# Kernel tuning notes

Measured on AMD Instinct MI355X. Metric: run time of the kernel, lower is better.

## Reference

```python
import jax, jax.numpy as jnp
import numpy as np

THRESHOLD = 0.5
NEGPOS_RATIO = 3
VARIANCES = (0.1, 0.2)

B, P, C, T = 64, 24564, 81, 50


def point_form(boxes):
    # center form (cx,cy,w,h) -> corner form (x1,y1,x2,y2)
    return jnp.concatenate([boxes[:, :2] - boxes[:, 2:] / 2,
                            boxes[:, :2] + boxes[:, 2:] / 2], axis=-1)


def jaccard(box_a, box_b):
    # box_a [T,4], box_b [P,4], corner form -> IoU [T,P]
    max_xy = jnp.minimum(box_a[:, None, 2:], box_b[None, :, 2:])
    min_xy = jnp.maximum(box_a[:, None, :2], box_b[None, :, :2])
    inter = jnp.prod(jnp.clip(max_xy - min_xy, 0.0), axis=-1)
    area_a = jnp.prod(box_a[:, 2:] - box_a[:, :2], axis=-1)[:, None]
    area_b = jnp.prod(box_b[:, 2:] - box_b[:, :2], axis=-1)[None, :]
    return inter / (area_a + area_b - inter)


def encode(matched, priors, variances):
    # matched [P,4] corner form, priors [P,4] center form
    g_cxcy = (matched[:, :2] + matched[:, 2:]) / 2 - priors[:, :2]
    g_cxcy = g_cxcy / (variances[0] * priors[:, 2:])
    g_wh = (matched[:, 2:] - matched[:, :2]) / priors[:, 2:]
    g_wh = jnp.log(g_wh) / variances[1]
    return jnp.concatenate([g_cxcy, g_wh], axis=-1)


def match_one(truths, labels, priors):
    # truths [T,4] corner, labels [T] int, priors [P,4] center form
    overlaps = jaccard(truths, point_form(priors))          # [T,P]
    best_prior_idx = jnp.argmax(overlaps, axis=1)           # [T] best prior per gt
    best_truth_overlap = jnp.max(overlaps, axis=0)          # [P]
    best_truth_idx = jnp.argmax(overlaps, axis=0)           # [P]
    # ensure every gt keeps its best prior
    best_truth_overlap = best_truth_overlap.at[best_prior_idx].set(2.0)
    best_truth_idx = best_truth_idx.at[best_prior_idx].set(jnp.arange(truths.shape[0]))
    matched = truths[best_truth_idx]                        # [P,4]
    conf = labels[best_truth_idx] + 1                       # background = 0
    conf = jnp.where(best_truth_overlap < THRESHOLD, 0, conf)
    loc = encode(matched, priors, VARIANCES)                # [P,4]
    return loc, conf


def setup_inputs() -> dict:
    key = jax.random.key(0)
    k1, k2, k3, k4, k5, k6, k7 = jax.random.split(key, 7)
    loc_data = jax.random.normal(k1, (B, P, 4), jnp.float32)
    conf_data = jax.random.normal(k2, (B, P, C), jnp.float32)
    # priors: center form, in-bounds
    ctr = 0.05 + 0.9 * jax.random.uniform(k3, (P, 2))
    wh = 0.05 + 0.25 * jax.random.uniform(k4, (P, 2))
    priors = jnp.concatenate([ctr, wh], axis=-1).astype(jnp.float32)
    # gt boxes: corner form with x2>x1, y2>y1
    xy1 = 0.7 * jax.random.uniform(k5, (B, T, 2))
    gwh = 0.05 + 0.25 * jax.random.uniform(k6, (B, T, 2))
    targets_boxes = jnp.concatenate([xy1, jnp.minimum(xy1 + gwh, 1.0)], axis=-1).astype(jnp.float32)
    targets_labels = jax.random.randint(k7, (B, T), 0, C - 1, jnp.int32)
    return {"loc_data": loc_data, "conf_data": conf_data, "priors": priors,
            "targets_boxes": targets_boxes, "targets_labels": targets_labels}


def reference(loc_data, conf_data, priors, targets_boxes, targets_labels):
    num, num_priors, _ = loc_data.shape
    # per-image matching, batched with vmap
    loc_t, conf_t = jax.vmap(lambda t, l: match_one(t, l, priors))(targets_boxes, targets_labels)
    pos = conf_t > 0                                         # [B,P]
    # localization: smooth-L1 over positives, sum
    diff = loc_data - loc_t
    ad = jnp.abs(diff)
    sl1 = jnp.where(ad < 1.0, 0.5 * diff * diff, ad - 0.5)
    loss_l = jnp.sum(sl1 * pos[..., None])
    # confidence: cross entropy = logsumexp - gathered logit
    logsm = jax.nn.log_softmax(conf_data, axis=-1)
    ce = -jnp.take_along_axis(logsm, conf_t[..., None], axis=-1)[..., 0]  # [B,P]
    # hard negative mining: rank losses among negatives
    loss_mine = jnp.where(pos, 0.0, ce)
    num_pos = jnp.sum(pos, axis=1)                           # [B]
    num_neg = jnp.minimum(NEGPOS_RATIO * num_pos, num_priors - 1)
    idx_rank = jnp.argsort(jnp.argsort(-loss_mine, axis=1), axis=1)
    neg = idx_rank < num_neg[:, None]
    loss_c = jnp.sum(jnp.where(pos | neg, ce, 0.0))
    n = jnp.maximum(jnp.sum(num_pos), 1).astype(loc_data.dtype)
    return jnp.stack([loss_l / n, loss_c / n])
```

## Files before the change

kernel.cpp:

```cpp
#include <hip/hip_runtime.h>
#include <cstdint>
#include <cstddef>

#define NB 64
#define NP 24564
#define NC 81
#define NROWS (NB*NP)
#define NT 50
#define TCH 10
#define NSEG 16
#define SEGLEN 1536

__device__ __forceinline__ unsigned long long umax64(unsigned long long a, unsigned long long b){
  return a > b ? a : b;
}

__global__ __launch_bounds__(256) void k_bestprior(
    const float* __restrict__ priors, const float* __restrict__ tboxes,
    unsigned long long* __restrict__ bpk)
{
  __shared__ float tb[TCH*4];
  __shared__ float ta[TCH];
  __shared__ unsigned long long part[4][TCH];
  const int tid = threadIdx.x;
  const int b  = blockIdx.x;
  const int t0 = blockIdx.y * TCH;
  const int i0 = blockIdx.z * SEGLEN;
  const int iend = min(i0 + SEGLEN, NP);
  if (tid < TCH*4) tb[tid] = tboxes[(b*NT + t0)*4 + tid];
  __syncthreads();
  if (tid < TCH) ta[tid] = (tb[tid*4+2]-tb[tid*4+0]) * (tb[tid*4+3]-tb[tid*4+1]);
  __syncthreads();

  unsigned long long best[TCH];
  #pragma unroll
  for (int j = 0; j < TCH; ++j) best[j] = 0ULL;

  for (int i = i0 + tid; i < iend; i += 256){
    const float4 pr = ((const float4* __restrict__)priors)[i];
    const float px1 = pr.x - 0.5f*pr.z, py1 = pr.y - 0.5f*pr.w;
    const float px2 = pr.x + 0.5f*pr.z, py2 = pr.y + 0.5f*pr.w;
    const float pa  = pr.z * pr.w;
    const unsigned long long low = (unsigned long long)(~(unsigned)i);
    #pragma unroll
    for (int j = 0; j < TCH; ++j){
      float ix = fminf(tb[j*4+2], px2) - fmaxf(tb[j*4+0], px1);
      float iy = fminf(tb[j*4+3], py2) - fmaxf(tb[j*4+1], py1);
      ix = fmaxf(ix, 0.0f); iy = fmaxf(iy, 0.0f);
      const float inter = ix * iy;
      const float iou = inter / (ta[j] + pa - inter);
      const unsigned long long key =
          ((unsigned long long)__float_as_uint(iou) << 32) | low;
      best[j] = umax64(best[j], key);
    }
  }
  #pragma unroll
  for (int off = 32; off > 0; off >>= 1){
    #pragma unroll
    for (int j = 0; j < TCH; ++j)
      best[j] = umax64(best[j], __shfl_down(best[j], off));
  }
  const int wv = tid >> 6;
  if ((tid & 63) == 0){
    #pragma unroll
    for (int j = 0; j < TCH; ++j) part[wv][j] = best[j];
  }
  __syncthreads();
  if (tid < TCH){
    const unsigned long long m =
        umax64(umax64(part[0][tid], part[1][tid]),
               umax64(part[2][tid], part[3][tid]));
    atomicMax(&bpk[b*NT + t0 + tid], m);
  }
}

__global__ __launch_bounds__(256) void k_ce(
    const float* __restrict__ conf, const float* __restrict__ loc,
    const float* __restrict__ priors, const float* __restrict__ tboxes,
    const int* __restrict__ tlabels,
    const unsigned long long* __restrict__ bpk,
    float* __restrict__ mine, float* __restrict__ ce_pos,
    float* __restrict__ loss_l, int* __restrict__ num_pos)
{
  __shared__ float tb[NT*4];
  __shared__ float ta[NT];
  __shared__ int ips[NT];
  __shared__ int tl[NT];
  const int tid = threadIdx.x;
  const int b = blockIdx.y;
  if (tid < NT*4) tb[tid] = tboxes[b*NT*4 + tid];
  else if (tid < NT*4 + NT){
    const int t = tid - NT*4;
    ips[t] = (int)(~(unsigned)(bpk[b*NT + t] & 0xffffffffULL));
  }
  __syncthreads();
  if (tid < NT){
    ta[tid] = (tb[tid*4+2]-tb[tid*4+0]) * (tb[tid*4+3]-tb[tid*4+1]);
    tl[tid] = tlabels[b*NT + tid];
  }
  __syncthreads();

  const int p0 = blockIdx.x*256 + tid;
  const bool active = p0 < NP;
  const int p = active ? p0 : (NP - 1);
  const int r = b*NP + p;
  const size_t e0 = (size_t)r * NC;
  const size_t a0 = e0 & ~(size_t)3;
  const int s = (int)(e0 & 3);

  const float4* __restrict__ c4 = (const float4* __restrict__)conf + (a0 >> 2);
  float4 w[21];
  #pragma unroll
  for (int j = 0; j < 21; ++j) w[j] = c4[j];

  const float4 pr = ((const float4* __restrict__)priors)[p];
  const float px1 = pr.x - 0.5f*pr.z, py1 = pr.y - 0.5f*pr.w;
  const float px2 = pr.x + 0.5f*pr.z, py2 = pr.y + 0.5f*pr.w;
  const float pa  = pr.z * pr.w;
  float ov = -1.0f; int ti = 0;
  for (int t = 0; t < NT; ++t){
    float ix = fminf(tb[t*4+2], px2) - fmaxf(tb[t*4+0], px1);
    float iy = fminf(tb[t*4+3], py2) - fmaxf(tb[t*4+1], py1);
    ix = fmaxf(ix, 0.0f); iy = fmaxf(iy, 0.0f);
    const float inter = ix * iy;
    const float iou = inter / (ta[t] + pa - inter);
    if (iou > ov){ ov = iou; ti = t; }
  }
  #pragma unroll 10
  for (int t = 0; t < NT; ++t){
    if (ips[t] == p){ ov = 2.0f; ti = t; }
  }
  const int cls = (ov < 0.5f) ? 0 : (tl[ti] + 1);

  const float NI = -INFINITY;
  const int idx = s + cls;
  float lg = 0.0f;
  #pragma unroll
  for (int j = 0; j < 21; ++j){
    if ((idx >> 2) == j){
      const float4 t4 = w[j];
      const int q = idx & 3;
      lg = (q == 0) ? t4.x : (q == 1) ? t4.y : (q == 2) ? t4.z : t4.w;
    }
  }
  w[0].x  = (s > 0) ? NI : w[0].x;
  w[0].y  = (s > 1) ? NI : w[0].y;
  w[0].z  = (s > 2) ? NI : w[0].z;
  w[20].y = (s < 1) ? NI : w[20].y;
  w[20].z = (s < 2) ? NI : w[20].z;
  w[20].w = (s < 3) ? NI : w[20].w;

  float m = w[0].w;
  #pragma unroll
  for (int j = 0; j < 21; ++j)
    m = fmaxf(m, fmaxf(fmaxf(w[j].x, w[j].y), fmaxf(w[j].z, w[j].w)));

  float s0 = 0.f, s1 = 0.f, s2 = 0.f, s3 = 0.f;
  #pragma unroll
  for (int j = 0; j < 21; ++j){
    s0 += __expf(w[j].x - m);
    s1 += __expf(w[j].y - m);
    s2 += __expf(w[j].z - m);
    s3 += __expf(w[j].w - m);
  }
  const float ce = m + __logf((s0 + s1) + (s2 + s3)) - lg;

  const bool pos = active && (cls > 0);
  if (active) mine[r] = pos ? 0.0f : ce;

  float cp = pos ? ce : 0.0f;
  float ll = 0.0f;
  int   pc = pos ? 1 : 0;
  if (pos){
    const float tx1 = tb[ti*4+0], ty1 = tb[ti*4+1], tx2 = tb[ti*4+2], ty2 = tb[ti*4+3];
    const float gcx = ((tx1 + tx2)*0.5f - pr.x) / (0.1f*pr.z);
    const float gcy = ((ty1 + ty2)*0.5f - pr.y) / (0.1f*pr.w);
    const float gw  = __logf((tx2 - tx1) / pr.z) * 5.0f;
    const float gh  = __logf((ty2 - ty1) / pr.w) * 5.0f;
    const float4 ld = ((const float4* __restrict__)loc)[r];
    float d, ad;
    d = ld.x - gcx; ad = fabsf(d); ll += (ad < 1.0f) ? 0.5f*d*d : ad - 0.5f;
    d = ld.y - gcy; ad = fabsf(d); ll += (ad < 1.0f) ? 0.5f*d*d : ad - 0.5f;
    d = ld.z - gw;  ad = fabsf(d); ll += (ad < 1.0f) ? 0.5f*d*d : ad - 0.5f;
    d = ld.w - gh;  ad = fabsf(d); ll += (ad < 1.0f) ? 0.5f*d*d : ad - 0.5f;
  }

  #pragma unroll
  for (int off = 32; off > 0; off >>= 1){
    cp += __shfl_down(cp, off);
    ll += __shfl_down(ll, off);
    pc += __shfl_down(pc, off);
  }
  __shared__ float rcp[4], rll[4];
  __shared__ int rpc[4];
  const int wv = tid >> 6;
  if ((tid & 63) == 0){ rcp[wv] = cp; rll[wv] = ll; rpc[wv] = pc; }
  __syncthreads();
  if (tid == 0){
    atomicAdd(&ce_pos[b], (rcp[0]+rcp[1])+(rcp[2]+rcp[3]));
    atomicAdd(&loss_l[b], (rll[0]+rll[1])+(rll[2]+rll[3]));
    atomicAdd(&num_pos[b], (rpc[0]+rpc[1])+(rpc[2]+rpc[3]));
  }
}

__global__ __launch_bounds__(1024) void k_topk(
    const float* __restrict__ mine, const int* __restrict__ num_pos,
    float* __restrict__ topk)
{
  const int b = blockIdx.x;
  const int tid = threadIdx.x;
  const float4* __restrict__ d4 =
      (const float4* __restrict__)(mine + (size_t)b * NP);
  const int k = min(3 * num_pos[b], NP - 1);

  __shared__ unsigned hist[256];
  __shared__ unsigned s_prefix;
  __shared__ int s_rem;
  __shared__ float wsum[16];

  if (k <= 0){
    if (tid == 0) topk[b] = 0.0f;
    return;
  }
  if (tid == 0){ s_prefix = 0u; s_rem = k; }

  for (int pass = 0; pass < 4; ++pass){
    const int shift = 24 - pass*8;
    if (tid < 256) hist[tid] = 0u;
    __syncthreads();
    const unsigned pref = s_prefix;
    const int rem = s_rem;
    for (int i = tid; i < 6141; i += 1024){
      const float4 v = d4[i];
      unsigned u;
      u = __float_as_uint(v.x);
      if (pass == 0 || (u >> (shift+8)) == pref) atomicAdd(&hist[(u>>shift)&255u], 1u);
      u = __float_as_uint(v.y);
      if (pass == 0 || (u >> (shift+8)) == pref) atomicAdd(&hist[(u>>shift)&255u], 1u);
      u = __float_as_uint(v.z);
      if (pass == 0 || (u >> (shift+8)) == pref) atomicAdd(&hist[(u>>shift)&255u], 1u);
      u = __float_as_uint(v.w);
      if (pass == 0 || (u >> (shift+8)) == pref) atomicAdd(&hist[(u>>shift)&255u], 1u);
    }
    __syncthreads();
    if (tid < 64){
      const unsigned h0 = hist[4*tid], h1 = hist[4*tid+1];
      const unsigned h2 = hist[4*tid+2], h3 = hist[4*tid+3];
      const unsigned pl = h0 + h1 + h2 + h3;
      unsigned S = pl;
      #pragma unroll
      for (int off = 1; off < 64; off <<= 1){
        const unsigned v = __shfl_down(S, off);
        if (tid + off < 64) S += v;
      }
      const unsigned Sn = S - pl;
      const unsigned t3 = h3 + Sn;
      const unsigned t2 = h2 + t3;
      const unsigned t1 = h1 + t2;
      const unsigned t0 = h0 + t1;
      if ((int)t0 >= rem && (int)t1 < rem){ s_prefix = (pref<<8) | (4u*tid+0u); s_rem = rem - (int)t1; }
      if ((int)t1 >= rem && (int)t2 < rem){ s_prefix = (pref<<8) | (4u*tid+1u); s_rem = rem - (int)t2; }
      if ((int)t2 >= rem && (int)t3 < rem){ s_prefix = (pref<<8) | (4u*tid+2u); s_rem = rem - (int)t3; }
      if ((int)t3 >= rem && (int)Sn < rem){ s_prefix = (pref<<8) | (4u*tid+3u); s_rem = rem - (int)Sn; }
    }
    __syncthreads();
  }

  const unsigned kb = s_prefix;
  const int rem = s_rem;
  const float kv = __uint_as_float(kb);
  float acc = 0.0f;
  for (int i = tid; i < 6141; i += 1024){
    const float4 v = d4[i];
    if (__float_as_uint(v.x) > kb) acc += v.x;
    if (__float_as_uint(v.y) > kb) acc += v.y;
    if (__float_as_uint(v.z) > kb) acc += v.z;
    if (__float_as_uint(v.w) > kb) acc += v.w;
  }
  #pragma unroll
  for (int off = 32; off > 0; off >>= 1) acc += __shfl_down(acc, off);
  if ((tid & 63) == 0) wsum[tid >> 6] = acc;
  __syncthreads();
  if (tid == 0){
    float s = 0.0f;
    #pragma unroll
    for (int j = 0; j < 16; ++j) s += wsum[j];
    topk[b] = s + (float)rem * kv;
  }
}

__global__ void k_final(const int* __restrict__ num_pos,
                        const float* __restrict__ loss_l,
                        const float* __restrict__ ce_pos,
                        const float* __restrict__ topk,
                        float* __restrict__ out)
{
  const int tid = threadIdx.x;
  int   np = num_pos[tid];
  float ll = loss_l[tid];
  float cp = ce_pos[tid];
  float tk = topk[tid];
  #pragma unroll
  for (int off = 32; off > 0; off >>= 1){
    np += __shfl_down(np, off);
    ll += __shfl_down(ll, off);
    cp += __shfl_down(cp, off);
    tk += __shfl_down(tk, off);
  }
  if (tid == 0){
    const float n = (float)max(np, 1);
    out[0] = ll / n;
    out[1] = (cp + tk) / n;
  }
}

extern "C" void kernel_launch(void* const* d_in, const int* in_sizes, int n_in,
                              void* d_out, int out_size, void* d_ws, size_t ws_size,
                              hipStream_t stream)
{
  const float* loc     = (const float*)d_in[0];
  const float* conf    = (const float*)d_in[1];
  const float* priors  = (const float*)d_in[2];
  const float* tboxes  = (const float*)d_in[3];
  const int*   tlabels = (const int*)d_in[4];
  float* out = (float*)d_out;

  char* ws = (char*)d_ws;
  int*   num_pos = (int*)(ws + 0);
  float* loss_l  = (float*)(ws + 256);
  float* ce_pos  = (float*)(ws + 512);
  float* topk    = (float*)(ws + 768);
  unsigned long long* bpk = (unsigned long long*)(ws + 1024);
  float* mine = (float*)(ws + 26624);

  hipMemsetAsync(ws, 0, 26624, stream);

  dim3 gA(NB, NT/TCH, NSEG);
  k_bestprior<<<gA, 256, 0, stream>>>(priors, tboxes, bpk);

  dim3 gC((NP + 255)/256, NB);
  k_ce<<<gC, 256, 0, stream>>>(conf, loc, priors, tboxes, tlabels,
                               bpk, mine, ce_pos, loss_l, num_pos);

  k_topk<<<NB, 1024, 0, stream>>>(mine, num_pos, topk);

  k_final<<<1, 64, 0, stream>>>(num_pos, loss_l, ce_pos, topk, out);
}
```

Baseline: 784.5 us.

## Stage conf rows in LDS with coalesced loads, split each row across two threads

The cross-entropy kernel now copies a block of 128 conf rows into shared memory with coalesced float4 loads, instead of each thread reading its own 324-byte row with strided vector loads. Each row is then handled by two threads, each covering half the classes, and the max and sum-exp are combined with lane shuffles. This is meant to improve global-memory coalescing and shorten the per-thread softmax chain. In exchange the IoU matching loop is computed redundantly by both threads of each row. The roughly 41 KB of LDS per block also limits how many blocks fit on a CU.

New measurement: 896.6 us. +14.3%, slower.

```diff
diff --git a/kernel.cpp b/kernel.cpp
--- a/kernel.cpp
+++ b/kernel.cpp
@@ -10,6 +10,7 @@
 #define TCH 10
 #define NSEG 16
 #define SEGLEN 1536
+#define RPB 128
 
 __device__ __forceinline__ unsigned long long umax64(unsigned long long a, unsigned long long b){
   return a > b ? a : b;
@@ -82,17 +83,28 @@
     float* __restrict__ mine, float* __restrict__ ce_pos,
     float* __restrict__ loss_l, int* __restrict__ num_pos)
 {
+  __shared__ float4 cbuf4[(RPB*NC)/4];
   __shared__ float tb[NT*4];
   __shared__ float ta[NT];
   __shared__ int ips[NT];
   __shared__ int tl[NT];
+  float* cbuf = (float*)cbuf4;
+
   const int tid = threadIdx.x;
-  const int b = blockIdx.y;
+  const int b  = blockIdx.y;
+  const int p0 = blockIdx.x * RPB;
+  const int rows = min(RPB, NP - p0);
+
   if (tid < NT*4) tb[tid] = tboxes[b*NT*4 + tid];
   else if (tid < NT*4 + NT){
     const int t = tid - NT*4;
     ips[t] = (int)(~(unsigned)(bpk[b*NT + t] & 0xffffffffULL));
   }
+
+  const float4* __restrict__ csrc =
+      (const float4* __restrict__)(conf + (size_t)(b*NP + p0) * NC);
+  const int nf4 = (rows * NC) >> 2;
+  for (int i = tid; i < nf4; i += 256) cbuf4[i] = csrc[i];
   __syncthreads();
   if (tid < NT){
     ta[tid] = (tb[tid*4+2]-tb[tid*4+0]) * (tb[tid*4+3]-tb[tid*4+1]);
@@ -100,18 +112,11 @@
   }
   __syncthreads();
 
-  const int p0 = blockIdx.x*256 + tid;
-  const bool active = p0 < NP;
-  const int p = active ? p0 : (NP - 1);
+  const int row = tid >> 1;
+  const int h   = tid & 1;
+  const bool active = row < rows;
+  const int p = p0 + (active ? row : 0);
   const int r = b*NP + p;
-  const size_t e0 = (size_t)r * NC;
-  const size_t a0 = e0 & ~(size_t)3;
-  const int s = (int)(e0 & 3);
-
-  const float4* __restrict__ c4 = (const float4* __restrict__)conf + (a0 >> 2);
-  float4 w[21];
-  #pragma unroll
-  for (int j = 0; j < 21; ++j) w[j] = c4[j];
 
   const float4 pr = ((const float4* __restrict__)priors)[p];
   const float px1 = pr.x - 0.5f*pr.z, py1 = pr.y - 0.5f*pr.w;
@@ -132,41 +137,29 @@
   }
   const int cls = (ov < 0.5f) ? 0 : (tl[ti] + 1);
 
-  const float NI = -INFINITY;
-  const int idx = s + cls;
-  float lg = 0.0f;
-  #pragma unroll
-  for (int j = 0; j < 21; ++j){
-    if ((idx >> 2) == j){
-      const float4 t4 = w[j];
-      const int q = idx & 3;
-      lg = (q == 0) ? t4.x : (q == 1) ? t4.y : (q == 2) ? t4.z : t4.w;
-    }
-  }
-  w[0].x  = (s > 0) ? NI : w[0].x;
-  w[0].y  = (s > 1) ? NI : w[0].y;
-  w[0].z  = (s > 2) ? NI : w[0].z;
-  w[20].y = (s < 1) ? NI : w[20].y;
-  w[20].z = (s < 2) ? NI : w[20].z;
-  w[20].w = (s < 3) ? NI : w[20].w;
-
-  float m = w[0].w;
-  #pragma unroll
-  for (int j = 0; j < 21; ++j)
-    m = fmaxf(m, fmaxf(fmaxf(w[j].x, w[j].y), fmaxf(w[j].z, w[j].w)));
-
-  float s0 = 0.f, s1 = 0.f, s2 = 0.f, s3 = 0.f;
-  #pragma unroll
-  for (int j = 0; j < 21; ++j){
-    s0 += __expf(w[j].x - m);
-    s1 += __expf(w[j].y - m);
-    s2 += __expf(w[j].z - m);
-    s3 += __expf(w[j].w - m);
-  }
-  const float ce = m + __logf((s0 + s1) + (s2 + s3)) - lg;
-
-  const bool pos = active && (cls > 0);
-  if (active) mine[r] = pos ? 0.0f : ce;
+  const float* __restrict__ myrow = cbuf + row * NC;
+  const int c0 = 41 * h;
+  float v[41];
+  #pragma unroll
+  for (int c = 0; c < 40; ++c) v[c] = myrow[c0 + c];
+  v[40] = h ? -INFINITY : myrow[40];
+
+  float mh = v[0];
+  #pragma unroll
+  for (int c = 1; c < 41; ++c) mh = fmaxf(mh, v[c]);
+  const float m = fmaxf(mh, __shfl_xor(mh, 1));
+
+  float sh = 0.0f;
+  #pragma unroll
+  for (int c = 0; c < 41; ++c) sh += __expf(v[c] - m);
+  const float S = sh + __shfl_xor(sh, 1);
+
+  const float lg = myrow[cls];
+  const float ce = m + __logf(S) - lg;
+
+  const bool own = active && (h == 0);
+  const bool pos = own && (cls > 0);
+  if (own) mine[r] = pos ? 0.0f : ce;
 
   float cp = pos ? ce : 0.0f;
   float ll = 0.0f;
@@ -338,7 +331,7 @@
   dim3 gA(NB, NT/TCH, NSEG);
   k_bestprior<<<gA, 256, 0, stream>>>(priors, tboxes, bpk);
 
-  dim3 gC((NP + 255)/256, NB);
+  dim3 gC((NP + RPB - 1)/RPB, NB);
   k_ce<<<gC, 256, 0, stream>>>(conf, loc, priors, tboxes, tlabels,
                                bpk, mine, ce_pos, loss_l, num_pos);
 
```
